# Optimization experiments

Measured on AMD Instinct MI355X. Metric: run time of the kernel, lower is better.

Reference implementation:

```python
import jax, jax.numpy as jnp
import numpy as np

B, N, C = 2, 2048, 1024
H = 16
R = 4
MLP = 4096
LORA_SCALE = 1.0 / R  # lora_alpha=1, r=4
EPS = 1e-5


def _ln(x, g, b):
    m = jnp.mean(x, axis=-1, keepdims=True)
    v = jnp.mean(jnp.square(x - m), axis=-1, keepdims=True)
    return (x - m) * jax.lax.rsqrt(v + EPS) * g + b


def setup_inputs() -> dict:
    key = jax.random.key(0)
    ks = jax.random.split(key, 16)
    s = lambda k, shape, fan: jax.random.normal(k, shape, jnp.float32) * (1.0 / np.sqrt(fan))
    return {
        "x": jax.random.normal(ks[0], (B, N, C), jnp.float32),
        "pos": jax.random.normal(ks[1], (B, N, C), jnp.float32),
        "Wqkv": s(ks[2], (3 * C, C), C),
        "b_qkv": jnp.zeros((3 * C,), jnp.float32),
        "lora_A": s(ks[3], (2 * R, C), C),          # rows 0:R -> q, R:2R -> v
        "lora_B": s(ks[4], (2 * C, R), R) * 0.1,     # rows 0:C -> q, C:2C -> v
        "Wproj": s(ks[5], (C, C), C),
        "b_proj": jnp.zeros((C,), jnp.float32),
        "ln1_g": jnp.ones((C,), jnp.float32),
        "ln1_b": jnp.zeros((C,), jnp.float32),
        "ln2_g": jnp.ones((C,), jnp.float32),
        "ln2_b": jnp.zeros((C,), jnp.float32),
        "W1": s(ks[6], (MLP, C), C),
        "b1": jnp.zeros((MLP,), jnp.float32),
        "W2": s(ks[7], (C, MLP), MLP),
        "b2": jnp.zeros((C,), jnp.float32),
        "idx": 0,
    }


def reference(x, pos, Wqkv, b_qkv, lora_A, lora_B, Wproj, b_proj,
              ln1_g, ln1_b, ln2_g, ln2_b, W1, b1, W2, b2, idx):
    # (dropout layers are identity in eval mode)
    x = x + pos

    # --- attention block: Residual(PreNormDrop(SelfAttention)) ---
    h = _ln(x, ln1_g, ln1_b)                              # [B,N,C]
    qkv = h @ Wqkv.T + b_qkv                              # [B,N,3C]
    # LoRA MergedLinear: low-rank update on q and v thirds only
    after_A = h @ lora_A.T                                # [B,N,2R]
    dq = after_A[..., :R] @ lora_B[:C].T * LORA_SCALE     # [B,N,C]
    dv = after_A[..., R:] @ lora_B[C:].T * LORA_SCALE     # [B,N,C]
    qkv = qkv.at[..., :C].add(dq).at[..., 2 * C:].add(dv)

    Dh = C // H
    q, k, v = [t.reshape(B, N, H, Dh).transpose(0, 2, 1, 3)
               for t in jnp.split(qkv, 3, axis=-1)]       # each [B,H,N,Dh]
    scale = Dh ** -0.5
    attn = jnp.einsum('bhid,bhjd->bhij', q, k) * scale    # [B,H,N,N]
    attn = jax.nn.softmax(attn, axis=-1)
    o = jnp.einsum('bhij,bhjd->bhid', attn, v)            # [B,H,N,Dh]
    o = o.transpose(0, 2, 1, 3).reshape(B, N, C)
    o = o @ Wproj.T + b_proj
    x = x + o

    # --- FFN block: Residual(PreNorm(FeedForward)) ---
    h2 = _ln(x, ln2_g, ln2_b)
    h2 = jax.nn.gelu(h2 @ W1.T + b1, approximate=False)
    h2 = h2 @ W2.T + b2
    return x + h2
```

## Files before the change

kernel.cpp:

```cpp
#include <hip/hip_runtime.h>
#include <hip/hip_bf16.h>
#include <math.h>

typedef __hip_bfloat16 bf16;
typedef __attribute__((ext_vector_type(4))) float f32x4;
typedef __attribute__((ext_vector_type(16))) float f32x16;
typedef __attribute__((ext_vector_type(8))) short s16x8;

__device__ __forceinline__ void async_cp16(void* lds, const void* g) {
    __builtin_amdgcn_global_load_lds((const __attribute__((address_space(1))) void*)g,
                                     (__attribute__((address_space(3))) void*)lds, 16, 0, 0);
}

__device__ __forceinline__ float gelu_fast(float x) {
    float y = 1.5957691216f * (x + 0.044715f * x * x * x);
    float t = __expf(y);
    float th = 1.0f - 2.0f / (t + 1.0f);
    return 0.5f * x * (1.0f + th);
}

__global__ __launch_bounds__(256)
void cvt_all(const float* __restrict__ w0, const float* __restrict__ w1,
             const float* __restrict__ w2, const float* __restrict__ w3,
             bf16* __restrict__ o0, bf16* __restrict__ o1,
             bf16* __restrict__ o2, bf16* __restrict__ o3) {
    int i = blockIdx.x * 256 + threadIdx.x;
    const float* src; bf16* dst; int j = i;
    if (j < 786432)            { src = w0; dst = o0; }
    else if (j < 1048576)      { j -= 786432;  src = w1; dst = o1; }
    else if (j < 2097152)      { j -= 1048576; src = w2; dst = o2; }
    else                       { j -= 2097152; src = w3; dst = o3; }
    float4 v = ((const float4*)src)[j];
    union { bf16 o[4]; uint2 u; } pk;
    pk.o[0] = __float2bfloat16(v.x); pk.o[1] = __float2bfloat16(v.y);
    pk.o[2] = __float2bfloat16(v.z); pk.o[3] = __float2bfloat16(v.w);
    ((uint2*)dst)[j] = pk.u;
}

template <bool ADD>
__global__ __launch_bounds__(256)
void ln_kernel(const float* __restrict__ xin, const float* __restrict__ pos,
               const float* __restrict__ gam, const float* __restrict__ bet,
               float* __restrict__ x1, bf16* __restrict__ hout) {
    const int row = blockIdx.x, tid = threadIdx.x;
    const size_t off = (size_t)row * 1024;
    float4 v = ((const float4*)(xin + off))[tid];
    if constexpr (ADD) {
        float4 p = ((const float4*)(pos + off))[tid];
        v.x += p.x; v.y += p.y; v.z += p.z; v.w += p.w;
        ((float4*)(x1 + off))[tid] = v;
    }
    float s  = v.x + v.y + v.z + v.w;
    float s2 = v.x*v.x + v.y*v.y + v.z*v.z + v.w*v.w;
#pragma unroll
    for (int o = 32; o >= 1; o >>= 1) { s += __shfl_xor(s, o); s2 += __shfl_xor(s2, o); }
    __shared__ float sS[4], sS2[4];
    int w = tid >> 6, lane = tid & 63;
    if (lane == 0) { sS[w] = s; sS2[w] = s2; }
    __syncthreads();
    float mean = (sS[0] + sS[1] + sS[2] + sS[3]) * (1.f / 1024.f);
    float e2   = (sS2[0] + sS2[1] + sS2[2] + sS2[3]) * (1.f / 1024.f);
    float rstd = rsqrtf(e2 - mean * mean + 1e-5f);
    float4 gv = ((const float4*)gam)[tid], bv = ((const float4*)bet)[tid];
    bf16* ho = hout + off + tid * 4;
    ho[0] = __float2bfloat16((v.x - mean) * rstd * gv.x + bv.x);
    ho[1] = __float2bfloat16((v.y - mean) * rstd * gv.y + bv.y);
    ho[2] = __float2bfloat16((v.z - mean) * rstd * gv.z + bv.z);
    ho[3] = __float2bfloat16((v.w - mean) * rstd * gv.w + bv.w);
}

template <int MODE>
__global__ __launch_bounds__(512, 2)
void gemm_bk64(const bf16* __restrict__ A, const bf16* __restrict__ B,
               const float* __restrict__ bias, bf16* __restrict__ outp,
               int M, int N, int K, int gx) {
    __shared__ bf16 As[2][256 * 64];
    __shared__ bf16 Bs[2][256 * 64];
    const int tid = threadIdx.x;
    const int lane = tid & 63, w = tid >> 6;
    const int grp = lane >> 4, c16 = lane & 15;
    const int wm = (w & 1) * 128, wn = (w >> 1) * 64;
    const int nwg = gridDim.x, bid = blockIdx.x;
    const int sw = (bid & 7) * (nwg >> 3) + (bid >> 3);
    const int bm = (sw / gx) * 256, bn = (sw % gx) * 256;

    f32x4 acc[8][4];
    const f32x4 zero = {0.f, 0.f, 0.f, 0.f};
#pragma unroll
    for (int mi = 0; mi < 8; mi++)
#pragma unroll
        for (int ni = 0; ni < 4; ni++) acc[mi][ni] = zero;

#define STAGE256(bufi, k0)                                                          \
    {                                                                               \
        const int buf_ = (bufi);                                                    \
        const int koff_ = (k0);                                                     \
        _Pragma("unroll") for (int t_ = 0; t_ < 4; t_++) {                          \
            int s_ = t_ * 512 + tid;                                                \
            int row_ = s_ >> 3, db_ = s_ & 7;                                       \
            int gb_ = (db_ ^ (row_ & 7)) << 3;                                      \
            async_cp16(&As[buf_][s_ * 8], A + (size_t)(bm + row_) * K + koff_ + gb_); \
            async_cp16(&Bs[buf_][s_ * 8], B + (size_t)(bn + row_) * K + koff_ + gb_); \
        }                                                                           \
    }

#define COMPUTE256(bufi)                                                            \
    {                                                                               \
        const int buf_ = (bufi);                                                    \
        _Pragma("unroll") for (int kc_ = 0; kc_ < 2; kc_++) {                       \
            s16x8 af_[8], bfv_[4];                                                  \
            _Pragma("unroll") for (int mi_ = 0; mi_ < 8; mi_++) {                   \
                int r_ = wm + mi_ * 16 + c16;                                       \
                af_[mi_] = *(const s16x8*)&As[buf_][r_ * 64 + ((((kc_ << 2) | grp) ^ (r_ & 7)) << 3)]; \
            }                                                                       \
            _Pragma("unroll") for (int ni_ = 0; ni_ < 4; ni_++) {                   \
                int r_ = wn + ni_ * 16 + c16;                                       \
                bfv_[ni_] = *(const s16x8*)&Bs[buf_][r_ * 64 + ((((kc_ << 2) | grp) ^ (r_ & 7)) << 3)]; \
            }                                                                       \
            _Pragma("unroll") for (int mi_ = 0; mi_ < 8; mi_++)                     \
                _Pragma("unroll") for (int ni_ = 0; ni_ < 4; ni_++)                 \
                    acc[mi_][ni_] = __builtin_amdgcn_mfma_f32_16x16x32_bf16(af_[mi_], bfv_[ni_], acc[mi_][ni_], 0, 0, 0); \
        }                                                                           \
    }

#define WAITV8 asm volatile("s_waitcnt vmcnt(8)" ::: "memory")
#define WAITV0 asm volatile("s_waitcnt vmcnt(0)" ::: "memory")

#define STEP256(BQ, TQ)                                                             \
    {                                                                               \
        const int tq_ = (TQ);                                                       \
        COMPUTE256(BQ);                                                             \
        __builtin_amdgcn_s_barrier();            \
        if (tq_ + 2 < nk) { STAGE256(BQ, (tq_ + 2) << 6); WAITV8; }                 \
        else { WAITV0; }                                \
        __builtin_amdgcn_s_barrier();             \
    }

    const int nk = K >> 6;
    STAGE256(0, 0);
    STAGE256(1, 64);
    WAITV8;
    __builtin_amdgcn_s_barrier();

    for (int t = 0; t < nk - 2; t += 2) {
        STEP256(0, t);
        STEP256(1, t + 1);
    }
    STEP256(0, nk - 2);
    COMPUTE256(1);

#undef STEP256
#undef WAITV8
#undef WAITV0
#undef STAGE256
#undef COMPUTE256

#pragma unroll
    for (int mi = 0; mi < 8; mi++)
#pragma unroll
        for (int ni = 0; ni < 4; ni++) {
            int r0 = bm + wm + mi * 16 + grp * 4;
            int c  = bn + wn + ni * 16 + c16;
            float bv = bias[c];
#pragma unroll
            for (int q = 0; q < 4; q++) {
                size_t idx = (size_t)(r0 + q) * N + c;
                float v = acc[mi][ni][q] + bv;
                if constexpr (MODE == 2) v = gelu_fast(v);
                outp[idx] = __float2bfloat16(v);
            }
        }
}

__global__ __launch_bounds__(256)
void gemm_n64(const bf16* __restrict__ A, const bf16* __restrict__ B,
              const float* __restrict__ bias, const float* __restrict__ resid,
              float* __restrict__ outp, int M, int N, int K, int gx) {
    __shared__ bf16 As[3][128 * 64];
    __shared__ bf16 Bs[3][64 * 64];
    const int tid = threadIdx.x;
    const int lane = tid & 63, w = tid >> 6;
    const int grp = lane >> 4, c16 = lane & 15;
    const int wm = w * 32;
    const int nwg = gridDim.x, bid = blockIdx.x;
    const int sw = (bid & 7) * (nwg >> 3) + (bid >> 3);
    const int bm = (sw / gx) * 128, bn = (sw % gx) * 64;

    f32x4 acc[2][4];
    const f32x4 zero = {0.f, 0.f, 0.f, 0.f};
#pragma unroll
    for (int mi = 0; mi < 2; mi++)
#pragma unroll
        for (int ni = 0; ni < 4; ni++) acc[mi][ni] = zero;

#define STAGE64(bufi, k0)                                                           \
    {                                                                               \
        const int buf_ = (bufi);                                                    \
        const int koff_ = (k0);                                                     \
        _Pragma("unroll") for (int t_ = 0; t_ < 4; t_++) {                          \
            int s_ = t_ * 256 + tid;                                                \
            int row_ = s_ >> 3, db_ = s_ & 7;                                       \
            async_cp16(&As[buf_][s_ * 8], A + (size_t)(bm + row_) * K + koff_ + ((db_ ^ (row_ & 7)) << 3)); \
        }                                                                           \
        _Pragma("unroll") for (int t_ = 0; t_ < 2; t_++) {                          \
            int s_ = t_ * 256 + tid;                                                \
            int row_ = s_ >> 3, db_ = s_ & 7;                                       \
            async_cp16(&Bs[buf_][s_ * 8], B + (size_t)(bn + row_) * K + koff_ + ((db_ ^ (row_ & 7)) << 3)); \
        }                                                                           \
    }

#define COMPUTE64(bufi)                                                             \
    {                                                                               \
        const int buf_ = (bufi);                                                    \
        _Pragma("unroll") for (int kc_ = 0; kc_ < 2; kc_++) {                       \
            s16x8 af_[2], bfv_[4];                                                  \
            _Pragma("unroll") for (int mi_ = 0; mi_ < 2; mi_++) {                   \
                int r_ = wm + mi_ * 16 + c16;                                       \
                af_[mi_] = *(const s16x8*)&As[buf_][r_ * 64 + ((((kc_ << 2) | grp) ^ (r_ & 7)) << 3)]; \
            }                                                                       \
            _Pragma("unroll") for (int ni_ = 0; ni_ < 4; ni_++) {                   \
                int rb_ = ni_ * 16 + c16;                                           \
                bfv_[ni_] = *(const s16x8*)&Bs[buf_][rb_ * 64 + ((((kc_ << 2) | grp) ^ (rb_ & 7)) << 3)]; \
            }                                                                       \
            _Pragma("unroll") for (int mi_ = 0; mi_ < 2; mi_++)                     \
                _Pragma("unroll") for (int ni_ = 0; ni_ < 4; ni_++)                 \
                    acc[mi_][ni_] = __builtin_amdgcn_mfma_f32_16x16x32_bf16(af_[mi_], bfv_[ni_], acc[mi_][ni_], 0, 0, 0); \
        }                                                                           \
    }

#define WAITV12 asm volatile("s_waitcnt vmcnt(12)" ::: "memory")
#define WAITV6  asm volatile("s_waitcnt vmcnt(6)"  ::: "memory")
#define WAITV0  asm volatile("s_waitcnt vmcnt(0)"  ::: "memory")

#define STEP64(BQ, TQ)                                                              \
    {                                                                               \
        const int tq_ = (TQ);                                                       \
        COMPUTE64(BQ);                                                              \
        __builtin_amdgcn_s_barrier();            \
        if (tq_ + 3 < nk) { STAGE64(BQ, (tq_ + 3) << 6); WAITV12; }                 \
        else if (tq_ + 2 < nk) { WAITV6; }                                          \
        else { WAITV0; }                                \
        __builtin_amdgcn_s_barrier();             \
    }

    const int nk = K >> 6;
    STAGE64(0, 0);
    STAGE64(1, 64);
    STAGE64(2, 128);
    WAITV12;
    __builtin_amdgcn_s_barrier();

    for (int t = 0; t < nk - 1; t += 3) {
        STEP64(0, t);
        STEP64(1, t + 1);
        STEP64(2, t + 2);
    }
    COMPUTE64(0);

#undef STEP64
#undef WAITV12
#undef WAITV6
#undef WAITV0
#undef STAGE64
#undef COMPUTE64

#pragma unroll
    for (int mi = 0; mi < 2; mi++)
#pragma unroll
        for (int ni = 0; ni < 4; ni++) {
            int r0 = bm + wm + mi * 16 + grp * 4;
            int c  = bn + ni * 16 + c16;
            float bv = bias[c];
#pragma unroll
            for (int q = 0; q < 4; q++) {
                size_t idx = (size_t)(r0 + q) * N + c;
                outp[idx] = acc[mi][ni][q] + bv + resid[idx];
            }
        }
}

__global__ __launch_bounds__(256)
void lora_a_kernel(const bf16* __restrict__ h, const float* __restrict__ A,
                   float* __restrict__ afterA) {
    const int row = blockIdx.x, tid = threadIdx.x;
    float hv[4];
#pragma unroll
    for (int t = 0; t < 4; t++) hv[t] = __bfloat162float(h[(size_t)row * 1024 + tid * 4 + t]);
    float p[8];
#pragma unroll
    for (int r = 0; r < 8; r++) {
        float4 av = ((const float4*)(A + (size_t)r * 1024))[tid];
        p[r] = hv[0] * av.x + hv[1] * av.y + hv[2] * av.z + hv[3] * av.w;
    }
#pragma unroll
    for (int r = 0; r < 8; r++)
#pragma unroll
        for (int o = 32; o >= 1; o >>= 1) p[r] += __shfl_xor(p[r], o);
    __shared__ float red[4][8];
    int w = tid >> 6, lane = tid & 63;
    if (lane == 0) {
#pragma unroll
        for (int r = 0; r < 8; r++) red[w][r] = p[r];
    }
    __syncthreads();
    if (tid < 8) afterA[(size_t)row * 8 + tid] = red[0][tid] + red[1][tid] + red[2][tid] + red[3][tid];
}

__global__ __launch_bounds__(256)
void attn_prep(const bf16* __restrict__ qkv, const float* __restrict__ afterA,
               const float* __restrict__ loraB, bf16* __restrict__ Qb,
               bf16* __restrict__ Kb, bf16* __restrict__ Vt) {
    const int bh = blockIdx.y, b = bh >> 4, h = bh & 15;
    const int it = blockIdx.x;
    __shared__ bf16 Vs[64 * 65];
    const int tid = threadIdx.x;
#pragma unroll
    for (int t = 0; t < 16; t++) {
        int s = t * 256 + tid;
        int il = s >> 6, d = s & 63;
        int ig = b * 2048 + it * 64 + il;
        size_t grow = (size_t)ig * 3072 + h * 64 + d;
        int col = h * 64 + d;
        const float* aA = afterA + (size_t)ig * 8;
        float4 bq = ((const float4*)loraB)[col];
        float4 bvv = ((const float4*)loraB)[1024 + col];
        float dq = (aA[0]*bq.x  + aA[1]*bq.y  + aA[2]*bq.z  + aA[3]*bq.w)  * 0.25f;
        float dv = (aA[4]*bvv.x + aA[5]*bvv.y + aA[6]*bvv.z + aA[7]*bvv.w) * 0.25f;
        float q = (__bfloat162float(qkv[grow]) + dq) * 0.18033688011f;
        float k = __bfloat162float(qkv[grow + 1024]);
        float v = __bfloat162float(qkv[grow + 2048]) + dv;
        size_t orow = (size_t)(bh * 2048 + it * 64 + il) * 64 + d;
        Qb[orow] = __float2bfloat16(q);
        Kb[orow] = __float2bfloat16(k);
        Vs[d * 65 + il] = __float2bfloat16(v);
    }
    __syncthreads();
#pragma unroll
    for (int t = 0; t < 16; t++) {
        int s = t * 256 + tid;
        int d = s >> 6, il = s & 63;
        Vt[(size_t)(bh * 64 + d) * 2048 + it * 64 + il] = Vs[d * 65 + il];
    }
}

__global__ __launch_bounds__(256)
void attn_fused(const bf16* __restrict__ Qb, const bf16* __restrict__ Kb,
                const bf16* __restrict__ Vt, bf16* __restrict__ Og) {
    __shared__ bf16 Qs[128 * 64], Ks[2][64 * 64], Vs[2][64 * 64];
    const int tid = threadIdx.x;
    const int lane = tid & 63, w = tid >> 6;
    const int c32 = lane & 31, l5 = lane >> 5;
    const int bid = blockIdx.x;
    const int sw = (bid & 7) * 64 + (bid >> 3);
    const int bh = sw >> 4, b = bh >> 4, h = bh & 15;
    const int i0 = (sw & 15) * 128;
    const int rowperm = (c32 & 19) | (((c32 >> 3) & 1) << 2) | (((c32 >> 2) & 1) << 3);

    const size_t qbase = (size_t)(bh * 2048 + i0) * 64;
    const size_t kbase = (size_t)bh * 2048 * 64;
    const size_t vbase = (size_t)bh * 64 * 2048;

#define STAGEKV(bufi, jv)                                                           \
    {                                                                               \
        const int buf_ = (bufi);                                                    \
        const int joff_ = (jv);                                                     \
        _Pragma("unroll") for (int t_ = 0; t_ < 2; t_++) {                          \
            int s_ = t_ * 256 + tid;                                                \
            int row_ = s_ >> 3, db_ = s_ & 7;                                       \
            int gb_ = (db_ ^ (row_ & 7)) << 3;                                      \
            async_cp16(&Ks[buf_][s_ * 8], Kb + kbase + (size_t)(joff_ + row_) * 64 + gb_); \
            async_cp16(&Vs[buf_][s_ * 8], Vt + vbase + (size_t)row_ * 2048 + joff_ + gb_); \
        }                                                                           \
    }

#pragma unroll
    for (int t = 0; t < 4; t++) {
        int s = t * 256 + tid;
        int row = s >> 3, db = s & 7;
        async_cp16(&Qs[s * 8], Qb + qbase + row * 64 + ((db ^ (row & 7)) << 3));
    }
    STAGEKV(0, 0);
    __syncthreads();

    s16x8 qf[4];
    {
        int rq = w * 32 + c32;
#pragma unroll
        for (int kc = 0; kc < 4; kc++) {
            int db = 2 * kc + l5;
            qf[kc] = *(const s16x8*)&Qs[rq * 64 + ((db ^ (rq & 7)) << 3)];
        }
    }

    f32x16 Oq[2];
#pragma unroll
    for (int dq = 0; dq < 2; dq++)
#pragma unroll
        for (int r = 0; r < 16; r++) Oq[dq][r] = 0.f;
    float l_lane = 0.f;

#define ATILE(BUF, JN)                                                              \
    {                                                                               \
        const int jn_ = (JN);                                                       \
        if (jn_ < 32) { STAGEKV((BUF) ^ 1, jn_ << 6); }                             \
        f32x16 Sq[2];                                                               \
        __builtin_amdgcn_s_setprio(1);                                              \
        _Pragma("unroll") for (int jq_ = 0; jq_ < 2; jq_++) {                       \
            _Pragma("unroll") for (int r_ = 0; r_ < 16; r_++) Sq[jq_][r_] = 0.f;    \
            int rk_ = jq_ * 32 + rowperm;                                           \
            _Pragma("unroll") for (int kc_ = 0; kc_ < 4; kc_++) {                   \
                int db_ = 2 * kc_ + l5;                                             \
                s16x8 af_ = *(const s16x8*)&Ks[BUF][rk_ * 64 + ((db_ ^ (rk_ & 7)) << 3)]; \
                Sq[jq_] = __builtin_amdgcn_mfma_f32_32x32x16_bf16(af_, qf[kc_], Sq[jq_], 0, 0, 0); \
            }                                                                       \
        }                                                                           \
        __builtin_amdgcn_s_setprio(0);                                              \
        s16x8 pf_[4];                                                               \
        _Pragma("unroll") for (int kc_ = 0; kc_ < 4; kc_++) {                       \
            union { s16x8 v; unsigned u4[4]; } u_;                                  \
            _Pragma("unroll") for (int pr_ = 0; pr_ < 4; pr_++) {                   \
                float a_ = Sq[kc_ >> 1][8 * (kc_ & 1) + 2 * pr_];                   \
                float b_ = Sq[kc_ >> 1][8 * (kc_ & 1) + 2 * pr_ + 1];               \
                float pa_, pb_;                                                     \
                asm("v_exp_f32 %0, %1" : "=v"(pa_) : "v"(a_));                      \
                asm("v_exp_f32 %0, %1" : "=v"(pb_) : "v"(b_));                      \
                l_lane += pa_; l_lane += pb_;                                       \
                unsigned pk_;                                                       \
                asm("v_cvt_pk_bf16_f32 %0, %1, %2" : "=v"(pk_) : "v"(pa_), "v"(pb_)); \
                u_.u4[pr_] = pk_;                                                   \
            }                                                                       \
            pf_[kc_] = u_.v;                                                        \
        }                                                                           \
        __builtin_amdgcn_s_setprio(1);                                              \
        _Pragma("unroll") for (int dq_ = 0; dq_ < 2; dq_++) {                       \
            int rd_ = dq_ * 32 + c32;                                               \
            _Pragma("unroll") for (int kc_ = 0; kc_ < 4; kc_++) {                   \
                int jb_ = 2 * kc_ + l5;                                             \
                s16x8 af_ = *(const s16x8*)&Vs[BUF][rd_ * 64 + ((jb_ ^ (rd_ & 7)) << 3)]; \
                Oq[dq_] = __builtin_amdgcn_mfma_f32_32x32x16_bf16(af_, pf_[kc_], Oq[dq_], 0, 0, 0); \
            }                                                                       \
        }                                                                           \
        __builtin_amdgcn_s_setprio(0);                                              \
        __syncthreads();                                                            \
    }

    for (int jt = 0; jt < 32; jt += 2) {
        ATILE(0, jt + 1);
        ATILE(1, jt + 2);
    }
#undef ATILE
#undef STAGEKV

    float l = l_lane + __shfl_xor(l_lane, 32);
    float inv = 1.0f / fmaxf(l, 1e-35f);
    int i = i0 + w * 32 + c32;
    size_t obase = (size_t)(b * 2048 + i) * 1024 + h * 64;
#pragma unroll
    for (int dq = 0; dq < 2; dq++)
#pragma unroll
        for (int rg = 0; rg < 4; rg++) {
            union { bf16 e[4]; uint2 u; } pk;
#pragma unroll
            for (int c = 0; c < 4; c++)
                pk.e[c] = __float2bfloat16(Oq[dq][rg * 4 + c] * inv);
            int d0 = dq * 32 + l5 * 4 + rg * 8;
            *(uint2*)&Og[obase + d0] = pk.u;
        }
}

extern "C" void kernel_launch(void* const* d_in, const int* in_sizes, int n_in,
                              void* d_out, int out_size, void* d_ws, size_t ws_size,
                              hipStream_t stream) {
    const float* x     = (const float*)d_in[0];
    const float* pos   = (const float*)d_in[1];
    const float* Wqkv  = (const float*)d_in[2];
    const float* bqkv  = (const float*)d_in[3];
    const float* loraA = (const float*)d_in[4];
    const float* loraB = (const float*)d_in[5];
    const float* Wproj = (const float*)d_in[6];
    const float* bproj = (const float*)d_in[7];
    const float* ln1g  = (const float*)d_in[8];
    const float* ln1b  = (const float*)d_in[9];
    const float* ln2g  = (const float*)d_in[10];
    const float* ln2b  = (const float*)d_in[11];
    const float* W1    = (const float*)d_in[12];
    const float* b1    = (const float*)d_in[13];
    const float* W2    = (const float*)d_in[14];
    const float* b2    = (const float*)d_in[15];

    char* ws = (char*)d_ws;
    float* x1     = (float*)(ws + 0);
    bf16*  hbuf   = (bf16*) (ws + 16777216);
    bf16*  qkv    = (bf16*) (ws + 25165824);
    bf16*  gbuf   = (bf16*) (ws + 50331648);
    float* afterA = (float*)(ws + 83886080);
    bf16*  Qb     = (bf16*) (ws + 84017152);
    bf16*  Kb     = (bf16*) (ws + 92405760);
    bf16*  Vt     = (bf16*) (ws + 100794368);
    bf16*  Obf    = (bf16*) (ws + 109182976);
    bf16*  Wqkvb  = (bf16*) (ws + 117571584);
    bf16*  Wprojb = (bf16*) (ws + 123863040);
    bf16*  W1b    = (bf16*) (ws + 125960192);
    bf16*  W2b    = (bf16*) (ws + 134348800);

    cvt_all<<<12288, 256, 0, stream>>>(Wqkv, Wproj, W1, W2, Wqkvb, Wprojb, W1b, W2b);

    ln_kernel<true><<<4096, 256, 0, stream>>>(x, pos, ln1g, ln1b, x1, hbuf);

    gemm_bk64<0><<<192, 512, 0, stream>>>(hbuf, Wqkvb, bqkv, qkv, 4096, 3072, 1024, 12);

    lora_a_kernel<<<4096, 256, 0, stream>>>(hbuf, loraA, afterA);

    attn_prep<<<dim3(32, 32), 256, 0, stream>>>(qkv, afterA, loraB, Qb, Kb, Vt);
    attn_fused<<<512, 256, 0, stream>>>(Qb, Kb, Vt, Obf);

    gemm_n64<<<512, 256, 0, stream>>>(Obf, Wprojb, bproj, x1, x1, 4096, 1024, 1024, 16);

    ln_kernel<false><<<4096, 256, 0, stream>>>(x1, nullptr, ln2g, ln2b, nullptr, hbuf);

    gemm_bk64<2><<<256, 512, 0, stream>>>(hbuf, W1b, b1, gbuf, 4096, 4096, 1024, 16);

    gemm_n64<<<512, 256, 0, stream>>>(gbuf, W2b, b2, x1, (float*)d_out, 4096, 1024, 4096, 16);

    (void)in_sizes; (void)n_in; (void)out_size; (void)ws_size;
}
```

Before: 370.2 us.

## Fuse LoRA update and Q/K/V head layout scatter into QKV GEMM epilogue

The QKV GEMM epilogue now applies the LoRA deltas to the q and v columns, scales q, and writes Q, K and transposed V directly into per-head buffers. This removes the separate attn_prep kernel and the intermediate qkv buffer round trip. LoRA-A is moved before the GEMM so afterA is ready for the epilogue. The epilogue stores are now scattered: Q and K writes are strided per element, while V writes are packed 4-wide along the sequence dimension.

```diff
diff --git a/kernel.cpp b/kernel.cpp
--- a/kernel.cpp
+++ b/kernel.cpp
@@ -73,6 +73,8 @@
 __global__ __launch_bounds__(512, 2)
 void gemm_bk64(const bf16* __restrict__ A, const bf16* __restrict__ B,
                const float* __restrict__ bias, bf16* __restrict__ outp,
+               const float* __restrict__ afterA, const float* __restrict__ loraB,
+               bf16* __restrict__ Qb, bf16* __restrict__ Kb, bf16* __restrict__ Vt,
                int M, int N, int K, int gx) {
     __shared__ bf16 As[2][256 * 64];
     __shared__ bf16 Bs[2][256 * 64];
@@ -155,21 +157,71 @@
 #undef STAGE256
 #undef COMPUTE256
 
-#pragma unroll
-    for (int mi = 0; mi < 8; mi++)
-#pragma unroll
-        for (int ni = 0; ni < 4; ni++) {
-            int r0 = bm + wm + mi * 16 + grp * 4;
-            int c  = bn + wn + ni * 16 + c16;
-            float bv = bias[c];
-#pragma unroll
-            for (int q = 0; q < 4; q++) {
-                size_t idx = (size_t)(r0 + q) * N + c;
-                float v = acc[mi][ni][q] + bv;
-                if constexpr (MODE == 2) v = gelu_fast(v);
-                outp[idx] = __float2bfloat16(v);
+    if constexpr (MODE == 1) {
+        const int role = bn >> 10;
+        const int g_b  = bm >> 11;
+#pragma unroll
+        for (int mi = 0; mi < 8; mi++) {
+            float4 aA4[4];
+            if (role != 1) {
+#pragma unroll
+                for (int q = 0; q < 4; q++) {
+                    int grow = bm + wm + mi * 16 + grp * 4 + q;
+                    aA4[q] = ((const float4*)afterA)[(size_t)grow * 2 + (role == 2 ? 1 : 0)];
+                }
+            }
+#pragma unroll
+            for (int ni = 0; ni < 4; ni++) {
+                int c  = bn + wn + ni * 16 + c16;
+                int cr = c & 1023;
+                int h  = cr >> 6, d = cr & 63;
+                float bv = bias[c];
+                if (role == 2) {
+                    float4 bw = ((const float4*)loraB)[1024 + cr];
+                    union { bf16 e[4]; uint2 u; } pk;
+#pragma unroll
+                    for (int q = 0; q < 4; q++) {
+                        float dv = (aA4[q].x*bw.x + aA4[q].y*bw.y + aA4[q].z*bw.z + aA4[q].w*bw.w) * 0.25f;
+                        pk.e[q] = __float2bfloat16(acc[mi][ni][q] + bv + dv);
+                    }
+                    int n0 = (bm & 2047) + wm + mi * 16 + grp * 4;
+                    *(uint2*)&Vt[((size_t)(g_b * 16 + h) * 64 + d) * 2048 + n0] = pk.u;
+                } else if (role == 0) {
+                    float4 bw = ((const float4*)loraB)[cr];
+#pragma unroll
+                    for (int q = 0; q < 4; q++) {
+                        int grow = bm + wm + mi * 16 + grp * 4 + q;
+                        float dq = (aA4[q].x*bw.x + aA4[q].y*bw.y + aA4[q].z*bw.z + aA4[q].w*bw.w) * 0.25f;
+                        float v = (acc[mi][ni][q] + bv + dq) * 0.18033688011f;
+                        Qb[((size_t)(g_b * 16 + h) * 2048 + (grow & 2047)) * 64 + d] = __float2bfloat16(v);
+                    }
+                } else {
+#pragma unroll
+                    for (int q = 0; q < 4; q++) {
+                        int grow = bm + wm + mi * 16 + grp * 4 + q;
+                        Kb[((size_t)(g_b * 16 + h) * 2048 + (grow & 2047)) * 64 + d] =
+                            __float2bfloat16(acc[mi][ni][q] + bv);
+                    }
+                }
             }
         }
+    } else {
+#pragma unroll
+        for (int mi = 0; mi < 8; mi++)
+#pragma unroll
+            for (int ni = 0; ni < 4; ni++) {
+                int r0 = bm + wm + mi * 16 + grp * 4;
+                int c  = bn + wn + ni * 16 + c16;
+                float bv = bias[c];
+#pragma unroll
+                for (int q = 0; q < 4; q++) {
+                    size_t idx = (size_t)(r0 + q) * N + c;
+                    float v = acc[mi][ni][q] + bv;
+                    if constexpr (MODE == 2) v = gelu_fast(v);
+                    outp[idx] = __float2bfloat16(v);
+                }
+            }
+    }
 }
 
 __global__ __launch_bounds__(256)
@@ -304,43 +356,6 @@
     }
     __syncthreads();
     if (tid < 8) afterA[(size_t)row * 8 + tid] = red[0][tid] + red[1][tid] + red[2][tid] + red[3][tid];
-}
-
-__global__ __launch_bounds__(256)
-void attn_prep(const bf16* __restrict__ qkv, const float* __restrict__ afterA,
-               const float* __restrict__ loraB, bf16* __restrict__ Qb,
-               bf16* __restrict__ Kb, bf16* __restrict__ Vt) {
-    const int bh = blockIdx.y, b = bh >> 4, h = bh & 15;
-    const int it = blockIdx.x;
-    __shared__ bf16 Vs[64 * 65];
-    const int tid = threadIdx.x;
-#pragma unroll
-    for (int t = 0; t < 16; t++) {
-        int s = t * 256 + tid;
-        int il = s >> 6, d = s & 63;
-        int ig = b * 2048 + it * 64 + il;
-        size_t grow = (size_t)ig * 3072 + h * 64 + d;
-        int col = h * 64 + d;
-        const float* aA = afterA + (size_t)ig * 8;
-        float4 bq = ((const float4*)loraB)[col];
-        float4 bvv = ((const float4*)loraB)[1024 + col];
-        float dq = (aA[0]*bq.x  + aA[1]*bq.y  + aA[2]*bq.z  + aA[3]*bq.w)  * 0.25f;
-        float dv = (aA[4]*bvv.x + aA[5]*bvv.y + aA[6]*bvv.z + aA[7]*bvv.w) * 0.25f;
-        float q = (__bfloat162float(qkv[grow]) + dq) * 0.18033688011f;
-        float k = __bfloat162float(qkv[grow + 1024]);
-        float v = __bfloat162float(qkv[grow + 2048]) + dv;
-        size_t orow = (size_t)(bh * 2048 + it * 64 + il) * 64 + d;
-        Qb[orow] = __float2bfloat16(q);
-        Kb[orow] = __float2bfloat16(k);
-        Vs[d * 65 + il] = __float2bfloat16(v);
-    }
-    __syncthreads();
-#pragma unroll
-    for (int t = 0; t < 16; t++) {
-        int s = t * 256 + tid;
-        int d = s >> 6, il = s & 63;
-        Vt[(size_t)(bh * 64 + d) * 2048 + it * 64 + il] = Vs[d * 65 + il];
-    }
 }
 
 __global__ __launch_bounds__(256)
@@ -491,7 +506,6 @@
     char* ws = (char*)d_ws;
     float* x1     = (float*)(ws + 0);
     bf16*  hbuf   = (bf16*) (ws + 16777216);
-    bf16*  qkv    = (bf16*) (ws + 25165824);
     bf16*  gbuf   = (bf16*) (ws + 50331648);
     float* afterA = (float*)(ws + 83886080);
     bf16*  Qb     = (bf16*) (ws + 84017152);
@@ -507,18 +521,21 @@
 
     ln_kernel<true><<<4096, 256, 0, stream>>>(x, pos, ln1g, ln1b, x1, hbuf);
 
-    gemm_bk64<0><<<192, 512, 0, stream>>>(hbuf, Wqkvb, bqkv, qkv, 4096, 3072, 1024, 12);
-
     lora_a_kernel<<<4096, 256, 0, stream>>>(hbuf, loraA, afterA);
 
-    attn_prep<<<dim3(32, 32), 256, 0, stream>>>(qkv, afterA, loraB, Qb, Kb, Vt);
+    gemm_bk64<1><<<192, 512, 0, stream>>>(hbuf, Wqkvb, bqkv, nullptr,
+                                          afterA, loraB, Qb, Kb, Vt,
+                                          4096, 3072, 1024, 12);
+
     attn_fused<<<512, 256, 0, stream>>>(Qb, Kb, Vt, Obf);
 
     gemm_n64<<<512, 256, 0, stream>>>(Obf, Wprojb, bproj, x1, x1, 4096, 1024, 1024, 16);
 
     ln_kernel<false><<<4096, 256, 0, stream>>>(x1, nullptr, ln2g, ln2b, nullptr, hbuf);
 
-    gemm_bk64<2><<<256, 512, 0, stream>>>(hbuf, W1b, b1, gbuf, 4096, 4096, 1024, 16);
+    gemm_bk64<2><<<256, 512, 0, stream>>>(hbuf, W1b, b1, gbuf,
+                                          nullptr, nullptr, nullptr, nullptr, nullptr,
+                                          4096, 4096, 1024, 16);
 
     gemm_n64<<<512, 256, 0, stream>>>(gbuf, W2b, b2, x1, (float*)d_out, 4096, 1024, 4096, 16);
 
```

Result: no change. 374.0 us (+1.0%).
